# Kernel optimization log

Measured on AMD Instinct MI355X. Metric: run time of the kernel, lower is better.

Reference implementation:

```python
import jax, jax.numpy as jnp
import numpy as np

B, S, C = 64, 2048, 128
P, Q = 4, 4


def setup_inputs() -> dict:
    key = jax.random.key(0)
    k1, k2, k3 = jax.random.split(key, 3)
    y = jax.random.normal(k1, (B, S, C), dtype=jnp.float32)
    # small positive coefficients keep the MA recurrence stable over S steps
    phi = 0.1 * jax.random.uniform(k2, (P,), dtype=jnp.float32)
    theta = 0.1 * jax.random.uniform(k3, (Q,), dtype=jnp.float32)
    sigma2 = jnp.ones((1,), dtype=jnp.float32)
    return {"y": y, "phi": phi, "theta": theta, "sigma2": sigma2}


def reference(y, phi, theta, sigma2):
    # ARIMA negative log-likelihood (arima_log_likelihood):
    #   e_t = y_t - sum_i phi_i * y_{t-i-1} - sum_j theta_j * e_{t-j-1}
    #   nll = -[ -0.5*S*log(2*pi*sigma2) - 0.5*sum(e^2)/sigma2 ]
    b, s, c = y.shape
    p = phi.shape[0]
    q = theta.shape[0]

    # AR part is a fixed causal convolution over the input -> precompute, vectorized.
    ypad = jnp.pad(y, ((0, 0), (p, 0), (0, 0)))  # zeros for t-i-1 < 0
    # lags[i, :, t, :] = y[:, t-i-1, :]   (zero when out of range)
    lags = jnp.stack([ypad[:, p - 1 - i: p - 1 - i + s, :] for i in range(p)], axis=0)
    z = y - jnp.einsum('i,ibsc->bsc', phi, lags)  # (B,S,C)

    # MA part is a true recurrence on the errors -> lax.scan over time.
    def step(carry, z_t):
        # carry: (q, B, C) = [e_{t-1}, e_{t-2}, ..., e_{t-q}] (most recent first)
        ma = jnp.einsum('j,jbc->bc', theta, carry)
        e_t = z_t - ma
        carry = jnp.concatenate([e_t[None], carry[:-1]], axis=0)
        return carry, e_t

    e0 = jnp.zeros((q, b, c), dtype=z.dtype)
    _, e = jax.lax.scan(step, e0, jnp.swapaxes(z, 0, 1))  # e: (S,B,C)

    ll = -0.5 * s * jnp.log(2.0 * jnp.pi * sigma2) - 0.5 * jnp.sum(e * e) / sigma2
    return -ll  # shape (1,)
```

## Files before the change

kernel.cpp:

```cpp
#include <hip/hip_runtime.h>
#include <math.h>

#define BB   64
#define SS   2048
#define CC   128
#define C2   (CC / 2)
#define LCH  128
#define NCH  (SS / LCH)
#define WARM 16
#define UNR  16
#define STEPS (WARM + LCH)
#define NBLK  (STEPS / UNR)
#define WBLK  (WARM / UNR)
#define GRID  (BB * NCH)

#define ARIMA_BATCH(SRC, ACCT)                                               \
    _Pragma("unroll")                                                        \
    for (int j = 0; j < UNR; ++j) {                                          \
        _Pragma("unroll")                                                    \
        for (int k = 0; k < 2; ++k) {                                        \
            const float y0 = SRC[j][k];                                      \
            const float z  = y0 - p1*Y1[k] - p2*Y2[k] - p3*Y3[k] - p4*Y4[k]; \
            const float e0 = z  - q2*E2[k] - q3*E3[k] - q4*E4[k] - q1*E1[k]; \
            if (ACCT) acc[k] += e0 * e0;                                     \
            Y4[k] = Y3[k]; Y3[k] = Y2[k]; Y2[k] = Y1[k]; Y1[k] = y0;         \
            E4[k] = E3[k]; E3[k] = E2[k]; E2[k] = E1[k]; E1[k] = e0;         \
        }                                                                    \
    }

__global__ void arima_init(const float* __restrict__ sigma2,
                           float* __restrict__ out)
{
    out[0] = 0.5f * (float)SS
           * logf(2.0f * 3.14159265358979323846f * sigma2[0]);
}

__global__ __launch_bounds__(64) void arima_main(
    const float2* __restrict__ yv,
    const float* __restrict__ phi,
    const float* __restrict__ theta,
    const float* __restrict__ sigma2,
    float* __restrict__ out)
{
    const int bid   = blockIdx.x;
    const int lane  = threadIdx.x;
    const int b     = bid >> 4;
    const int chunk = bid & 15;

    const float p1 = phi[0],   p2 = phi[1],   p3 = phi[2],   p4 = phi[3];
    const float q1 = theta[0], q2 = theta[1], q3 = theta[2], q4 = theta[3];

    const float2* base = yv + (size_t)b * SS * C2 + lane;
    const int t0 = chunk * LCH - WARM;

    float Y1[2] = {0,0}, Y2[2] = {0,0}, Y3[2] = {0,0}, Y4[2] = {0,0};
    float cur[UNR][2];
    if (chunk) {
        float2 v;
        v = base[(size_t)(t0-1) * C2]; Y1[0]=v.x; Y1[1]=v.y;
        v = base[(size_t)(t0-2) * C2]; Y2[0]=v.x; Y2[1]=v.y;
        v = base[(size_t)(t0-3) * C2]; Y3[0]=v.x; Y3[1]=v.y;
        v = base[(size_t)(t0-4) * C2]; Y4[0]=v.x; Y4[1]=v.y;
#pragma unroll
        for (int j = 0; j < UNR; ++j) {
            float2 w = base[(size_t)(t0 + j) * C2];
            cur[j][0] = w.x; cur[j][1] = w.y;
        }
    } else {
#pragma unroll
        for (int j = 0; j < UNR; ++j) { cur[j][0] = 0.f; cur[j][1] = 0.f; }
    }
    float E1[2] = {0,0}, E2[2] = {0,0}, E3[2] = {0,0}, E4[2] = {0,0};
    float acc[2] = {0,0};

    int tcur = t0 + UNR;
    for (int blk = 0; blk < NBLK - 1; ++blk) {
        float nxt[UNR][2];
#pragma unroll
        for (int j = 0; j < UNR; ++j) {
            float2 v = base[(size_t)(tcur + j) * C2];
            nxt[j][0] = v.x; nxt[j][1] = v.y;
        }
        tcur += UNR;
        const bool acct = (blk >= WBLK);
        ARIMA_BATCH(cur, acct)
#pragma unroll
        for (int j = 0; j < UNR; ++j) { cur[j][0] = nxt[j][0]; cur[j][1] = nxt[j][1]; }
    }
    ARIMA_BATCH(cur, true)

    float a = acc[0] + acc[1];
#pragma unroll
    for (int off = 32; off > 0; off >>= 1)
        a += __shfl_down(a, off, 64);
    if (lane == 0) {
        atomicAdd(out, 0.5f * a / sigma2[0]);
    }
}

extern "C" void kernel_launch(void* const* d_in, const int* in_sizes, int n_in,
                              void* d_out, int out_size, void* d_ws, size_t ws_size,
                              hipStream_t stream) {
    const float2* yv    = (const float2*)d_in[0];
    const float* phi    = (const float*)d_in[1];
    const float* theta  = (const float*)d_in[2];
    const float* sigma2 = (const float*)d_in[3];
    float* out = (float*)d_out;
    (void)d_ws; (void)ws_size;

    arima_init<<<1, 1, 0, stream>>>(sigma2, out);
    arima_main<<<GRID, 64, 0, stream>>>(yv, phi, theta, sigma2, out);
}
```

Baseline: 108.7 us.

## Split sequence into smaller chunks and preload whole chunk into registers

Chunk length drops from 128 to 32, so the grid grows fourfold to 4096 blocks of 64 threads. Each thread now loads its full 48-step window (16 warm-up steps plus 32) into registers up front, behind a scheduling barrier, instead of double-buffering 16-step batches. This is meant to raise parallelism and hide memory latency by issuing all loads at once. The cost is redundant warm-up work, rising from 16/144 to 16/48 of the steps, plus higher register pressure and four times as many atomics.

New measurement: 144.7 us. +33.2%, slower.

```diff
diff --git a/kernel.cpp b/kernel.cpp
--- a/kernel.cpp
+++ b/kernel.cpp
@@ -5,28 +5,11 @@
 #define SS   2048
 #define CC   128
 #define C2   (CC / 2)
-#define LCH  128
+#define LCH  32
 #define NCH  (SS / LCH)
 #define WARM 16
-#define UNR  16
 #define STEPS (WARM + LCH)
-#define NBLK  (STEPS / UNR)
-#define WBLK  (WARM / UNR)
 #define GRID  (BB * NCH)
-
-#define ARIMA_BATCH(SRC, ACCT)                                               \
-    _Pragma("unroll")                                                        \
-    for (int j = 0; j < UNR; ++j) {                                          \
-        _Pragma("unroll")                                                    \
-        for (int k = 0; k < 2; ++k) {                                        \
-            const float y0 = SRC[j][k];                                      \
-            const float z  = y0 - p1*Y1[k] - p2*Y2[k] - p3*Y3[k] - p4*Y4[k]; \
-            const float e0 = z  - q2*E2[k] - q3*E3[k] - q4*E4[k] - q1*E1[k]; \
-            if (ACCT) acc[k] += e0 * e0;                                     \
-            Y4[k] = Y3[k]; Y3[k] = Y2[k]; Y2[k] = Y1[k]; Y1[k] = y0;         \
-            E4[k] = E3[k]; E3[k] = E2[k]; E2[k] = E1[k]; E1[k] = e0;         \
-        }                                                                    \
-    }
 
 __global__ void arima_init(const float* __restrict__ sigma2,
                            float* __restrict__ out)
@@ -44,8 +27,8 @@
 {
     const int bid   = blockIdx.x;
     const int lane  = threadIdx.x;
-    const int b     = bid >> 4;
-    const int chunk = bid & 15;
+    const int b     = bid >> 6;
+    const int chunk = bid & 63;
 
     const float p1 = phi[0],   p2 = phi[1],   p3 = phi[2],   p4 = phi[3];
     const float q1 = theta[0], q2 = theta[1], q3 = theta[2], q4 = theta[3];
@@ -54,7 +37,7 @@
     const int t0 = chunk * LCH - WARM;
 
     float Y1[2] = {0,0}, Y2[2] = {0,0}, Y3[2] = {0,0}, Y4[2] = {0,0};
-    float cur[UNR][2];
+    float cur[STEPS][2];
     if (chunk) {
         float2 v;
         v = base[(size_t)(t0-1) * C2]; Y1[0]=v.x; Y1[1]=v.y;
@@ -62,32 +45,35 @@
         v = base[(size_t)(t0-3) * C2]; Y3[0]=v.x; Y3[1]=v.y;
         v = base[(size_t)(t0-4) * C2]; Y4[0]=v.x; Y4[1]=v.y;
 #pragma unroll
-        for (int j = 0; j < UNR; ++j) {
+        for (int j = 0; j < STEPS; ++j) {
             float2 w = base[(size_t)(t0 + j) * C2];
             cur[j][0] = w.x; cur[j][1] = w.y;
         }
     } else {
 #pragma unroll
-        for (int j = 0; j < UNR; ++j) { cur[j][0] = 0.f; cur[j][1] = 0.f; }
+        for (int j = 0; j < WARM; ++j) { cur[j][0] = 0.f; cur[j][1] = 0.f; }
+#pragma unroll
+        for (int j = WARM; j < STEPS; ++j) {
+            float2 w = base[(size_t)(t0 + j) * C2];
+            cur[j][0] = w.x; cur[j][1] = w.y;
+        }
     }
+    __builtin_amdgcn_sched_barrier(0);
+
     float E1[2] = {0,0}, E2[2] = {0,0}, E3[2] = {0,0}, E4[2] = {0,0};
     float acc[2] = {0,0};
-
-    int tcur = t0 + UNR;
-    for (int blk = 0; blk < NBLK - 1; ++blk) {
-        float nxt[UNR][2];
 #pragma unroll
-        for (int j = 0; j < UNR; ++j) {
-            float2 v = base[(size_t)(tcur + j) * C2];
-            nxt[j][0] = v.x; nxt[j][1] = v.y;
+    for (int j = 0; j < STEPS; ++j) {
+#pragma unroll
+        for (int k = 0; k < 2; ++k) {
+            const float y0 = cur[j][k];
+            const float z  = y0 - p1*Y1[k] - p2*Y2[k] - p3*Y3[k] - p4*Y4[k];
+            const float e0 = z  - q2*E2[k] - q3*E3[k] - q4*E4[k] - q1*E1[k];
+            if (j >= WARM) acc[k] += e0 * e0;
+            Y4[k] = Y3[k]; Y3[k] = Y2[k]; Y2[k] = Y1[k]; Y1[k] = y0;
+            E4[k] = E3[k]; E3[k] = E2[k]; E2[k] = E1[k]; E1[k] = e0;
         }
-        tcur += UNR;
-        const bool acct = (blk >= WBLK);
-        ARIMA_BATCH(cur, acct)
-#pragma unroll
-        for (int j = 0; j < UNR; ++j) { cur[j][0] = nxt[j][0]; cur[j][1] = nxt[j][1]; }
     }
-    ARIMA_BATCH(cur, true)
 
     float a = acc[0] + acc[1];
 #pragma unroll
```
